# Kernel optimization log

Hardware: AMD Instinct MI355X
Metric: run time of the kernel (lower is better)

Reference implementation:

```python
import jax, jax.numpy as jnp
import numpy as np

DIM = 4096
N_HEADS = 32
N_KV_HEADS = 8
HEAD_DIM = DIM // N_HEADS  # 128
N_REP = N_HEADS // N_KV_HEADS  # 4
FFN_HIDDEN = 11008
EPS = 1e-6
B, S = 4, 2048


def rms_norm(x, gamma):
    # x: [b, s, d]
    var = jnp.mean(x * x, axis=-1, keepdims=True)
    return gamma * (x * jax.lax.rsqrt(var + EPS))


def apply_rope(x, cos, sin):
    # x: [b, s, h, d]; cos/sin: [s, d/2]. Complex rotation on (even, odd) pairs.
    x2 = x.reshape(*x.shape[:-1], HEAD_DIM // 2, 2)
    x0, x1 = x2[..., 0], x2[..., 1]
    c = cos[None, :, None, :]
    s = sin[None, :, None, :]
    r0 = x0 * c - x1 * s
    r1 = x0 * s + x1 * c
    return jnp.stack([r0, r1], axis=-1).reshape(x.shape)


def setup_inputs() -> dict:
    key = jax.random.key(0)
    ks = jax.random.split(key, 16)
    sc = 0.02
    inp = {
        "x": jax.random.normal(ks[0], (B, S, DIM), dtype=jnp.float32),
        "freqs": jax.random.uniform(ks[1], (S, HEAD_DIM // 2), dtype=jnp.float32) * (2 * np.pi),
        "start_pos": 0,
        "gamma_attn": jnp.ones((DIM,), jnp.float32),
        "gamma_ffn": jnp.ones((DIM,), jnp.float32),
        "wq_w": sc * jax.random.normal(ks[2], (N_HEADS * HEAD_DIM, DIM), jnp.float32),
        "wq_b": jnp.zeros((N_HEADS * HEAD_DIM,), jnp.float32),
        "wk_w": sc * jax.random.normal(ks[3], (N_KV_HEADS * HEAD_DIM, DIM), jnp.float32),
        "wk_b": jnp.zeros((N_KV_HEADS * HEAD_DIM,), jnp.float32),
        "wv_w": sc * jax.random.normal(ks[4], (N_KV_HEADS * HEAD_DIM, DIM), jnp.float32),
        "wv_b": jnp.zeros((N_KV_HEADS * HEAD_DIM,), jnp.float32),
        "wo_w": sc * jax.random.normal(ks[5], (DIM, N_HEADS * HEAD_DIM), jnp.float32),
        "wo_b": jnp.zeros((DIM,), jnp.float32),
        "w1_w": sc * jax.random.normal(ks[6], (FFN_HIDDEN, DIM), jnp.float32),
        "w3_w": sc * jax.random.normal(ks[7], (FFN_HIDDEN, DIM), jnp.float32),
        "w2_w": sc * jax.random.normal(ks[8], (DIM, FFN_HIDDEN), jnp.float32),
    }
    return inp


def reference(x, freqs, start_pos, gamma_attn, gamma_ffn,
              wq_w, wq_b, wk_w, wk_b, wv_w, wv_b, wo_w, wo_b,
              w1_w, w3_w, w2_w):
    cos, sin = jnp.cos(freqs), jnp.sin(freqs)

    # --- attention sublayer ---
    xn = rms_norm(x, gamma_attn)
    xq = (xn @ wq_w.T + wq_b).reshape(B, S, N_HEADS, HEAD_DIM)
    xk = (xn @ wk_w.T + wk_b).reshape(B, S, N_KV_HEADS, HEAD_DIM)
    xv = (xn @ wv_w.T + wv_b).reshape(B, S, N_KV_HEADS, HEAD_DIM)
    xq = apply_rope(xq, cos, sin)
    xk = apply_rope(xk, cos, sin)

    # KV cache: start_pos=0 prefill -> cache slice [0:start_pos+S] == current xk/xv
    keys = jnp.repeat(xk, N_REP, axis=2)   # [b, s, n_heads, d]
    values = jnp.repeat(xv, N_REP, axis=2)

    scores = jnp.einsum('bqhd,bkhd->bhqk', xq, keys) / np.sqrt(HEAD_DIM)
    probs = jax.nn.softmax(scores.astype(jnp.float32), axis=-1).astype(xq.dtype)
    attn = jnp.einsum('bhqk,bkhd->bqhd', probs, values).reshape(B, S, DIM)
    h = x + attn @ wo_w.T + wo_b

    # --- FFN sublayer (LLaMA SwiGLU) ---
    hn = rms_norm(h, gamma_ffn)
    ff = (jax.nn.silu(hn @ w1_w.T) * (hn @ w3_w.T)) @ w2_w.T
    return h + ff
```

## Files before the change

### kernel.cpp

```cpp
#include <hip/hip_runtime.h>
#include <hip/hip_bf16.h>

#define DIM   4096
#define NH    32
#define NKV   8
#define HD    128
#define FFNH  11008
#define BATCH 4
#define SEQ   2048
#define MTOT  (BATCH*SEQ)

using bf16x8_t = __attribute__((ext_vector_type(8))) short;
using f32x4_t  = __attribute__((ext_vector_type(4))) float;

typedef const __attribute__((address_space(1))) unsigned int GlbU32;
typedef __attribute__((address_space(3))) unsigned int LdsU32;

__device__ __forceinline__ unsigned short f2b(float f) {
  union { float f; unsigned int u; } v; v.f = f;
  return (unsigned short)((v.u + 0x7fffu + ((v.u >> 16) & 1u)) >> 16);
}
__device__ __forceinline__ float b2f(unsigned short b) {
  union { unsigned int u; float f; } v; v.u = ((unsigned int)b) << 16;
  return v.f;
}
__device__ __forceinline__ void gll16(const void* g, void* l) {
  __builtin_amdgcn_global_load_lds((GlbU32*)g, (LdsU32*)l, 16, 0, 0);
}

#define VM8  asm volatile("s_waitcnt vmcnt(8)" ::: "memory")
#define VM4M asm volatile("s_waitcnt vmcnt(4)" ::: "memory")
#define VM0  asm volatile("s_waitcnt vmcnt(0)" ::: "memory")

__global__ __launch_bounds__(256)
void cvt_bf16_k(const float* __restrict__ src, unsigned short* __restrict__ dst)
{
  const size_t i = ((size_t)blockIdx.x * 256 + threadIdx.x) * 8;
  const float4 a = *(const float4*)&src[i];
  const float4 b = *(const float4*)&src[i + 4];
  union { int4 v; unsigned short u[8]; } o;
  o.u[0] = f2b(a.x); o.u[1] = f2b(a.y); o.u[2] = f2b(a.z); o.u[3] = f2b(a.w);
  o.u[4] = f2b(b.x); o.u[5] = f2b(b.y); o.u[6] = f2b(b.z); o.u[7] = f2b(b.w);
  *(int4*)&dst[i] = o.v;
}

__global__ __launch_bounds__(256)
void rmsnorm_k(const float* __restrict__ X, const float* __restrict__ gamma,
               unsigned short* __restrict__ Y)
{
  const int row = blockIdx.x, t = threadIdx.x;
  const float* xr = X + (size_t)row * DIM;
  float4 v[4];
  float ss = 0.f;
#pragma unroll
  for (int p = 0; p < 4; ++p) {
    v[p] = *(const float4*)&xr[p * 1024 + t * 4];
    ss += v[p].x*v[p].x + v[p].y*v[p].y + v[p].z*v[p].z + v[p].w*v[p].w;
  }
#pragma unroll
  for (int off = 32; off >= 1; off >>= 1) ss += __shfl_xor(ss, off, 64);
  __shared__ float red[4];
  if ((t & 63) == 0) red[t >> 6] = ss;
  __syncthreads();
  const float tot = red[0] + red[1] + red[2] + red[3];
  const float rn = rsqrtf(tot * (1.f / DIM) + 1e-6f);
  unsigned short* yr = Y + (size_t)row * DIM;
#pragma unroll
  for (int p = 0; p < 4; ++p) {
    const float4 gv = *(const float4*)&gamma[p * 1024 + t * 4];
    short4 o;
    o.x = (short)f2b(v[p].x * gv.x * rn);
    o.y = (short)f2b(v[p].y * gv.y * rn);
    o.z = (short)f2b(v[p].z * gv.z * rn);
    o.w = (short)f2b(v[p].w * gv.w * rn);
    *(short4*)&yr[p * 1024 + t * 4] = o;
  }
}

template<int NHT>
__global__ __launch_bounds__(256)
void rope_k(unsigned short* __restrict__ buf, const float* __restrict__ fr)
{
  const int u = blockIdx.x * 256 + threadIdx.x;
  const int per_row = NHT * 16;
  const int row  = u / per_row;
  const int rem  = u - row * per_row;
  const int head = rem >> 4;
  const int i4   = (rem & 15) << 2;
  const int s    = row & (SEQ - 1);
  unsigned short* p = buf + (size_t)row * (NHT * HD) + head * HD + i4 * 2;
  union { int4 v; unsigned short u16[8]; } d;
  d.v = *(const int4*)p;
  const float4 f = *(const float4*)&fr[s * 64 + i4];
  const float fa[4] = {f.x, f.y, f.z, f.w};
#pragma unroll
  for (int i = 0; i < 4; ++i) {
    float sn, c;
    __sincosf(fa[i], &sn, &c);
    const float x0 = b2f(d.u16[2*i]), x1 = b2f(d.u16[2*i+1]);
    d.u16[2*i]   = f2b(x0 * c - x1 * sn);
    d.u16[2*i+1] = f2b(x0 * sn + x1 * c);
  }
  *(int4*)p = d.v;
}

template<int MODE>
__global__ __launch_bounds__(512)
void gemm256(const unsigned short* __restrict__ A,
             const unsigned short* __restrict__ W,
             const unsigned short* __restrict__ W3p,
             const float* __restrict__ bias,
             const float* res,
             float* outF,
             unsigned short* __restrict__ outH,
             const unsigned short* __restrict__ wkp,
             const unsigned short* __restrict__ wvp,
             const float* __restrict__ bkp,
             const float* __restrict__ bvp,
             unsigned short* __restrict__ okp,
             unsigned short* __restrict__ ovp,
             int K)
{
  __shared__ __align__(16) char smem[131072];
  const int t = threadIdx.x, lane = t & 63, wid = t >> 6;
  const int wr = wid >> 2, wc = wid & 3;
  const int G = gridDim.x, bid = blockIdx.x;
  const int wg = (bid & 7) * (G >> 3) + (bid >> 3);
  const int NBN = G >> 5;
  const int span = NBN << 3;
  const int tmg = wg / span, rr = wg - tmg * span;
  const int tn = rr >> 3, tm = (tmg << 3) + (rr & 7);
  const int m0 = tm << 8;
  const int NSUB = K >> 5;

  const unsigned short *P1, *P2;
  const float* bp = bias;
  unsigned short* oh = outH;
  int nloc = 0, colsN = 4096;
  if constexpr (MODE == 0) {
    const int n0 = tn << 8;
    if (n0 < 4096)      { nloc = n0;        P1 = W   + (size_t)nloc * K; bp = bias; oh = outH; colsN = 4096; }
    else if (n0 < 5120) { nloc = n0 - 4096; P1 = wkp + (size_t)nloc * K; bp = bkp;  oh = okp;  colsN = 1024; }
    else                { nloc = n0 - 5120; P1 = wvp + (size_t)nloc * K; bp = bvp;  oh = ovp;  colsN = 1024; }
    P2 = P1 + (size_t)128 * K;
  } else if constexpr (MODE == 3) {
    const int n0w = tn << 7;
    P1 = W   + (size_t)n0w * K;
    P2 = W3p + (size_t)n0w * K;
    nloc = n0w;
  } else {
    const int n0 = tn << 8;
    P1 = W + (size_t)n0 * K;
    P2 = P1 + (size_t)128 * K;
    nloc = n0;
  }

  const int r0 = t >> 2, gg = t & 3;
  const int gsw = gg ^ ((r0 >> 1) & 3);

  auto stA = [&](int sig) {
    if (sig < NSUB) {
      const int slot = sig & 3;
      gll16(A + (size_t)(m0 + r0) * K + sig * 32 + gsw * 8,
            smem + slot * 16384 + wid * 1024);
      gll16(A + (size_t)(m0 + 128 + r0) * K + sig * 32 + gsw * 8,
            smem + slot * 16384 + 8192 + wid * 1024);
    }
  };
  auto stB = [&](int sig) {
    if (sig < NSUB) {
      const int slot = sig & 3;
      gll16(P1 + (size_t)r0 * K + sig * 32 + gsw * 8,
            smem + 65536 + slot * 16384 + wid * 1024);
      gll16(P2 + (size_t)r0 * K + sig * 32 + gsw * 8,
            smem + 65536 + slot * 16384 + 8192 + wid * 1024);
    }
  };
  auto rdA = [&](int slot, int mo) -> bf16x8_t {
    const int lrow = wr * 128 + mo + (lane & 15);
    const int g = (lane >> 4) ^ ((lrow >> 1) & 3);
    return *(const bf16x8_t*)(smem + slot * 16384 + lrow * 64 + g * 16);
  };
  auto rdB = [&](int slot, int nf) -> bf16x8_t {
    const int brow = wc * 64 + nf * 16 + (lane & 15);
    const int g = (lane >> 4) ^ ((brow >> 1) & 3);
    return *(const bf16x8_t*)(smem + 65536 + slot * 16384 + brow * 64 + g * 16);
  };

  f32x4_t acc[8][4];
#pragma unroll
  for (int i = 0; i < 8; ++i)
#pragma unroll
    for (int j = 0; j < 4; ++j) acc[i][j] = (f32x4_t)0.f;

  stA(0); stB(0); stA(1); stB(1); stA(2); stB(2);
  VM8;
  __builtin_amdgcn_s_barrier();

  for (int p = 0; p < NSUB; ++p) {
    const int slot = p & 3;
    bf16x8_t bfv[4], afv[8];
#pragma unroll
    for (int n = 0; n < 4; ++n) bfv[n] = rdB(slot, n);
#pragma unroll
    for (int m = 0; m < 8; ++m) afv[m] = rdA(slot, m * 16);
    stA(p + 3); stB(p + 3);
    __builtin_amdgcn_s_setprio(1);
#pragma unroll
    for (int m = 0; m < 8; ++m)
#pragma unroll
      for (int n = 0; n < 4; ++n)
        acc[m][n] = __builtin_amdgcn_mfma_f32_16x16x32_bf16(afv[m], bfv[n], acc[m][n], 0, 0, 0);
    __builtin_amdgcn_s_setprio(0);
    if (p < NSUB - 3)      { VM8; }
    else if (p == NSUB - 3){ VM4M; }
    else                   { VM0; }
    __builtin_amdgcn_s_barrier();
  }

  if constexpr (MODE == 0) {
#pragma unroll
    for (int ni = 0; ni < 4; ++ni) {
      const int col = nloc + wc * 64 + ni * 16 + (lane & 15);
      const float bv = bp[col];
#pragma unroll
      for (int mi = 0; mi < 8; ++mi)
#pragma unroll
        for (int r = 0; r < 4; ++r) {
          const int row = m0 + wr * 128 + mi * 16 + (lane >> 4) * 4 + r;
          oh[(size_t)row * colsN + col] = f2b(acc[mi][ni][r] + bv);
        }
    }
  } else if constexpr (MODE == 1 || MODE == 2) {
#pragma unroll
    for (int ni = 0; ni < 4; ++ni) {
      const int col = nloc + wc * 64 + ni * 16 + (lane & 15);
      float bv = 0.f;
      if constexpr (MODE == 1) bv = bias[col];
#pragma unroll
      for (int mi = 0; mi < 8; ++mi)
#pragma unroll
        for (int r = 0; r < 4; ++r) {
          const int row = m0 + wr * 128 + mi * 16 + (lane >> 4) * 4 + r;
          const size_t idx = (size_t)row * 4096 + col;
          outF[idx] = acc[mi][ni][r] + bv + res[idx];
        }
    }
  } else {
    if (wc >= 2) {
      const int widx = wr * 2 + (wc - 2);
#pragma unroll
      for (int ni = 0; ni < 4; ++ni)
#pragma unroll
        for (int mi = 0; mi < 8; ++mi)
#pragma unroll
          for (int r = 0; r < 4; ++r) {
            const int lrow = mi * 16 + (lane >> 4) * 4 + r;
            const int ncol = ni * 16 + (lane & 15);
            *(unsigned short*)(smem + widx * 16384 + lrow * 128 + ncol * 2) =
                f2b(acc[mi][ni][r]);
          }
    }
    __syncthreads();
    if (wc < 2) {
      const int widx = wr * 2 + wc;
#pragma unroll
      for (int ni = 0; ni < 4; ++ni)
#pragma unroll
        for (int mi = 0; mi < 8; ++mi)
#pragma unroll
          for (int r = 0; r < 4; ++r) {
            const int lrow = mi * 16 + (lane >> 4) * 4 + r;
            const int ncol = ni * 16 + (lane & 15);
            const float s3 = b2f(*(const unsigned short*)(smem + widx * 16384 + lrow * 128 + ncol * 2));
            const float s1 = acc[mi][ni][r];
            const float sig = 1.f / (1.f + __expf(-s1));
            const int row = m0 + wr * 128 + lrow;
            outH[(size_t)row * FFNH + nloc + wc * 64 + ncol] = f2b(s1 * sig * s3);
          }
    }
  }
}

__global__ __launch_bounds__(256, 3)
void attn_k(const unsigned short* __restrict__ Q, const unsigned short* __restrict__ Kb,
            const unsigned short* __restrict__ Vb, unsigned short* __restrict__ O,
            const float* __restrict__ woS, unsigned short* __restrict__ woD,
            const float* __restrict__ w1S, unsigned short* __restrict__ w1D,
            const float* __restrict__ w3S, unsigned short* __restrict__ w3D)
{
  __shared__ unsigned short Ks[4][4096];
  __shared__ unsigned short Vt[2][4096];
  __shared__ unsigned short Ps[2560];
  const int t = threadIdx.x, lane = t & 63, wid = t >> 6;
  const int bx = blockIdx.x;
  const int qt = bx & 31, h = (bx >> 5) & 31, b = bx >> 10;
  const int kvh = h >> 2;
  const float rs = 0.08838834764831845f;
  constexpr int NPAIR = SEQ / 64;

  const int q0 = wid * 16;
  const int qc = lane & 15;

  bf16x8_t qf[4];
  {
    const unsigned short* qrow = Q + (size_t)(b * SEQ + qt * 64 + q0 + qc) * DIM
                                   + h * HD + (lane >> 4) * 8;
#pragma unroll
    for (int ks = 0; ks < 4; ++ks) qf[ks] = *(const bf16x8_t*)(qrow + ks * 32);
  }

  const unsigned short* Kbase = Kb + (size_t)(b * SEQ) * (NKV * HD) + kvh * HD;
  const unsigned short* Vbase = Vb + (size_t)(b * SEQ) * (NKV * HD) + kvh * HD;

  auto stK = [&](int kt, int slot) {
#pragma unroll
    for (int oo = 0; oo < 2; ++oo) {
      const int o = wid * 2 + oo;
      const int row = o * 4 + (lane >> 4);
      const int gl  = (lane & 15) ^ (row & 7);
      gll16(Kbase + (size_t)(kt * 32 + row) * (NKV * HD) + gl * 8, &Ks[slot][o * 512]);
    }
  };
  const int kv = t >> 3, dc = (t & 7) << 4;
  const int colv = kv ^ ((t & 3) << 3);
  auto ldV = [&](int kt, int4& lo, int4& hi) {
    const unsigned short* gp = Vbase + (size_t)(kt * 32 + kv) * (NKV * HD) + dc;
    lo = *(const int4*)gp;
    hi = *(const int4*)(gp + 8);
  };
  auto wrV = [&](int slot, int4 vlo, int4 vhi) {
    union { int4 v; unsigned short u[8]; } lo, hi;
    lo.v = vlo; hi.v = vhi;
#pragma unroll
    for (int j = 0; j < 8; ++j) Vt[slot][(dc + j) * 32 + colv] = lo.u[j];
#pragma unroll
    for (int j = 0; j < 8; ++j) Vt[slot][(dc + 8 + j) * 32 + colv] = hi.u[j];
  };

  int4 a0l, a0h, a1l, a1h, b0l, b0h, b1l, b1h;
  stK(0, 0); ldV(0, a0l, a0h); stK(1, 1); ldV(1, a1l, a1h);
  stK(2, 2); ldV(2, b0l, b0h); stK(3, 3); ldV(3, b1l, b1h);

  f32x4_t oa[8];
#pragma unroll
  for (int i = 0; i < 8; ++i) oa[i] = (f32x4_t)0.f;
  float mrun = -1e30f, lrun = 0.f;
  const int pbase = wid * 640 + qc * 40;
  const int pwr   = pbase + (lane >> 4) * 4;

  auto pack2 = [&](float x, float y) -> unsigned int {
    return (unsigned int)f2b(x) | ((unsigned int)f2b(y) << 16);
  };

  auto pairIter = [&](int p, int sb, int4& l0, int4& h0, int4& l1, int4& h1) {
    if (p == NPAIR - 1) { VM0; } else { VM8; }
    wrV(0, l0, h0);
    wrV(1, l1, h1);
    asm volatile("s_waitcnt lgkmcnt(0)" ::: "memory");
    __builtin_amdgcn_s_barrier();

    f32x4_t st[4];
    st[0] = (f32x4_t)0.f; st[1] = (f32x4_t)0.f;
    st[2] = (f32x4_t)0.f; st[3] = (f32x4_t)0.f;
    const int kr0 = qc, kr1 = 16 + qc;
    __builtin_amdgcn_s_setprio(1);
#pragma unroll
    for (int ks = 0; ks < 4; ++ks) {
      const bf16x8_t k00 = *(const bf16x8_t*)&Ks[sb][(kr0 * 128 + ks * 32 + (lane >> 4) * 8) ^ ((kr0 & 7) << 3)];
      st[0] = __builtin_amdgcn_mfma_f32_16x16x32_bf16(k00, qf[ks], st[0], 0, 0, 0);
      const bf16x8_t k01 = *(const bf16x8_t*)&Ks[sb][(kr1 * 128 + ks * 32 + (lane >> 4) * 8) ^ ((kr1 & 7) << 3)];
      st[1] = __builtin_amdgcn_mfma_f32_16x16x32_bf16(k01, qf[ks], st[1], 0, 0, 0);
      const bf16x8_t k10 = *(const bf16x8_t*)&Ks[sb + 1][(kr0 * 128 + ks * 32 + (lane >> 4) * 8) ^ ((kr0 & 7) << 3)];
      st[2] = __builtin_amdgcn_mfma_f32_16x16x32_bf16(k10, qf[ks], st[2], 0, 0, 0);
      const bf16x8_t k11 = *(const bf16x8_t*)&Ks[sb + 1][(kr1 * 128 + ks * 32 + (lane >> 4) * 8) ^ ((kr1 & 7) << 3)];
      st[3] = __builtin_amdgcn_mfma_f32_16x16x32_bf16(k11, qf[ks], st[3], 0, 0, 0);
    }
    __builtin_amdgcn_s_setprio(0);

    float mx01 = fmaxf(fmaxf(st[0][0], st[0][1]), fmaxf(st[0][2], st[0][3]));
    float mx23 = fmaxf(fmaxf(st[1][0], st[1][1]), fmaxf(st[1][2], st[1][3]));
    float mx45 = fmaxf(fmaxf(st[2][0], st[2][1]), fmaxf(st[2][2], st[2][3]));
    float mx67 = fmaxf(fmaxf(st[3][0], st[3][1]), fmaxf(st[3][2], st[3][3]));
    float pm = fmaxf(fmaxf(mx01, mx23), fmaxf(mx45, mx67)) * rs;
    pm = fmaxf(pm, __shfl_xor(pm, 16, 64));
    pm = fmaxf(pm, __shfl_xor(pm, 32, 64));

    const int grow = __any(pm > mrun);
    if (grow) {
      const float mnew = fmaxf(mrun, pm);
      const float corr = __expf(mrun - mnew);
      mrun = mnew;
      lrun *= corr;
      float c4[4];
#pragma unroll
      for (int r = 0; r < 4; ++r) c4[r] = __shfl(corr, (lane >> 4) * 4 + r, 16);
#pragma unroll
      for (int i = 0; i < 8; ++i)
#pragma unroll
        for (int r = 0; r < 4; ++r) oa[i][r] *= c4[r];
    }

    float ssum = 0.f;
#pragma unroll
    for (int tt = 0; tt < 4; ++tt)
#pragma unroll
      for (int r = 0; r < 4; ++r) {
        st[tt][r] = __expf(st[tt][r] * rs - mrun);
        ssum += st[tt][r];
      }
    ssum += __shfl_xor(ssum, 16, 64);
    ssum += __shfl_xor(ssum, 32, 64);
    lrun += ssum;

    *(unsigned int*)&Ps[pwr]      = pack2(st[0][0], st[0][1]);
    *(unsigned int*)&Ps[pwr + 2]  = pack2(st[0][2], st[0][3]);
    *(unsigned int*)&Ps[pwr + 16] = pack2(st[1][0], st[1][1]);
    *(unsigned int*)&Ps[pwr + 18] = pack2(st[1][2], st[1][3]);
    const bf16x8_t pa0 = *(const bf16x8_t*)&Ps[pbase + (lane >> 4) * 8];
    asm volatile("s_waitcnt lgkmcnt(0)" ::: "memory");
    *(unsigned int*)&Ps[pwr]      = pack2(st[2][0], st[2][1]);
    *(unsigned int*)&Ps[pwr + 2]  = pack2(st[2][2], st[2][3]);
    *(unsigned int*)&Ps[pwr + 16] = pack2(st[3][0], st[3][1]);
    *(unsigned int*)&Ps[pwr + 18] = pack2(st[3][2], st[3][3]);
    const bf16x8_t pa1 = *(const bf16x8_t*)&Ps[pbase + (lane >> 4) * 8];

    __builtin_amdgcn_s_setprio(1);
#pragma unroll
    for (int nt2 = 0; nt2 < 8; ++nt2) {
      const bf16x8_t vf0 = *(const bf16x8_t*)&Vt[0][(nt2 * 16 + (lane & 15)) * 32 + (((lane >> 4) ^ (nt2 & 3)) << 3)];
      oa[nt2] = __builtin_amdgcn_mfma_f32_16x16x32_bf16(pa0, vf0, oa[nt2], 0, 0, 0);
      const bf16x8_t vf1 = *(const bf16x8_t*)&Vt[1][(nt2 * 16 + (lane & 15)) * 32 + (((lane >> 4) ^ (nt2 & 3)) << 3)];
      oa[nt2] = __builtin_amdgcn_mfma_f32_16x16x32_bf16(pa1, vf1, oa[nt2], 0, 0, 0);
    }
    __builtin_amdgcn_s_setprio(0);
    __builtin_amdgcn_s_barrier();
    if (p + 2 < NPAIR) {
      stK(2 * p + 4, sb);     ldV(2 * p + 4, l0, h0);
      stK(2 * p + 5, sb + 1); ldV(2 * p + 5, l1, h1);
    }
  };

  for (int j = 0; j < NPAIR / 2; ++j) {
    pairIter(2 * j,     0, a0l, a0h, a1l, a1h);
    pairIter(2 * j + 1, 2, b0l, b0h, b1l, b1h);
  }

  float inv[4];
#pragma unroll
  for (int r = 0; r < 4; ++r) inv[r] = 1.f / __shfl(lrun, (lane >> 4) * 4 + r, 16);
#pragma unroll
  for (int nt2 = 0; nt2 < 8; ++nt2) {
    const int col = h * HD + nt2 * 16 + (lane & 15);
#pragma unroll
    for (int r = 0; r < 4; ++r) {
      const int row = qt * 64 + q0 + (lane >> 4) * 4 + r;
      O[(size_t)(b * SEQ + row) * DIM + col] = f2b(oa[nt2][r] * inv[r]);
    }
  }

  {
    const size_t gt = (size_t)bx * 256 + t;
    for (size_t e = gt * 8; e < 106954752ull; e += 8ull * 1048576ull) {
      const float* src; unsigned short* dst; size_t o;
      if (e < 16777216ull)      { src = woS; dst = woD; o = e; }
      else if (e < 61865984ull) { src = w1S; dst = w1D; o = e - 16777216ull; }
      else                      { src = w3S; dst = w3D; o = e - 61865984ull; }
      const float4 va = *(const float4*)&src[o];
      const float4 vb = *(const float4*)&src[o + 4];
      union { int4 v; unsigned short u[8]; } ov;
      ov.u[0] = f2b(va.x); ov.u[1] = f2b(va.y); ov.u[2] = f2b(va.z); ov.u[3] = f2b(va.w);
      ov.u[4] = f2b(vb.x); ov.u[5] = f2b(vb.y); ov.u[6] = f2b(vb.z); ov.u[7] = f2b(vb.w);
      *(int4*)&dst[o] = ov.v;
    }
  }
}

extern "C" void kernel_launch(void* const* d_in, const int* in_sizes, int n_in,
                              void* d_out, int out_size, void* d_ws, size_t ws_size,
                              hipStream_t stream)
{
  (void)in_sizes; (void)n_in; (void)out_size; (void)ws_size;
  const float* x   = (const float*)d_in[0];
  const float* fr  = (const float*)d_in[1];
  const float* ga  = (const float*)d_in[3];
  const float* gf  = (const float*)d_in[4];
  const float* wq  = (const float*)d_in[5];
  const float* wqb = (const float*)d_in[6];
  const float* wk  = (const float*)d_in[7];
  const float* wkb = (const float*)d_in[8];
  const float* wv  = (const float*)d_in[9];
  const float* wvb = (const float*)d_in[10];
  const float* wo  = (const float*)d_in[11];
  const float* wob = (const float*)d_in[12];
  const float* w1  = (const float*)d_in[13];
  const float* w3  = (const float*)d_in[14];
  const float* w2  = (const float*)d_in[15];
  float* out = (float*)d_out;

  constexpr size_t MB = 1ull << 20;
  char* ws = (char*)d_ws;
  unsigned short* xn = (unsigned short*)(ws);
  unsigned short* qb = (unsigned short*)(ws + 64*MB);
  unsigned short* kb = (unsigned short*)(ws + 128*MB);
  unsigned short* vb = (unsigned short*)(ws + 144*MB);
  unsigned short* ao = (unsigned short*)(ws + 160*MB);
  unsigned short* hn = (unsigned short*)(ws + 224*MB);
  unsigned short* g  = (unsigned short*)(ws);
  unsigned short* wscr = (unsigned short*)(ws + 288*MB);
  unsigned short* wqB = wscr;
  unsigned short* wkB = wscr + 16*MB;
  unsigned short* wvB = wscr + 20*MB;
  unsigned short* woB = (unsigned short*)(ws);
  unsigned short* w1B = wscr;
  unsigned short* w3B = wscr + 46*MB;
  unsigned short* w2B = wscr;

  rmsnorm_k<<<MTOT, 256, 0, stream>>>(x, ga, xn);
  cvt_bf16_k<<<(NH*HD*DIM)/2048,  256, 0, stream>>>(wq, wqB);
  cvt_bf16_k<<<(NKV*HD*DIM)/2048, 256, 0, stream>>>(wk, wkB);
  cvt_bf16_k<<<(NKV*HD*DIM)/2048, 256, 0, stream>>>(wv, wvB);
  gemm256<0><<<(MTOT/256)*((DIM+2*NKV*HD)/256), 512, 0, stream>>>(
      xn, wqB, nullptr, wqb, nullptr, nullptr, qb,
      wkB, wvB, wkb, wvb, kb, vb, DIM);
  rope_k<NH><<<(MTOT*NH*16)/256,  256, 0, stream>>>(qb, fr);
  rope_k<NKV><<<(MTOT*NKV*16)/256,256, 0, stream>>>(kb, fr);
  attn_k<<<BATCH*NH*(SEQ/64), 256, 0, stream>>>(qb, kb, vb, ao,
      wo, woB, w1, w1B, w3, w3B);
  gemm256<1><<<(MTOT/256)*(DIM/256), 512, 0, stream>>>(
      ao, woB, nullptr, wob, x, out, nullptr,
      nullptr, nullptr, nullptr, nullptr, nullptr, nullptr, DIM);
  rmsnorm_k<<<MTOT, 256, 0, stream>>>(out, gf, hn);
  gemm256<3><<<(MTOT/256)*(FFNH/128), 512, 0, stream>>>(
      hn, w1B, w3B, nullptr, nullptr, nullptr, g,
      nullptr, nullptr, nullptr, nullptr, nullptr, nullptr, DIM);
  cvt_bf16_k<<<(FFNH*DIM)/2048, 256, 0, stream>>>(w2, w2B);
  gemm256<2><<<(MTOT/256)*(DIM/256), 512, 0, stream>>>(
      g, w2B, nullptr, nullptr, out, out, nullptr,
      nullptr, nullptr, nullptr, nullptr, nullptr, nullptr, FFNH);
}
```

Before: 3.632 ms.

## Double attention query tile to 128 rows with 8 waves per block

The attention kernel now runs 512 threads (8 waves) per block covering 128 query rows instead of 64, halving the grid. Each K/V tile loaded into shared memory is reused by twice as many query rows, which cuts global K/V traffic and per-block load work; the K/V staging is respread across 512 threads with one 16-byte load each. The cost is a larger P scratch buffer, fewer blocks to fill the GPU, and a tighter register budget under the new launch bound of 4 blocks.

```diff
diff --git a/kernel.cpp b/kernel.cpp
--- a/kernel.cpp
+++ b/kernel.cpp
@@ -282,7 +282,7 @@
   }
 }
 
-__global__ __launch_bounds__(256, 3)
+__global__ __launch_bounds__(512, 4)
 void attn_k(const unsigned short* __restrict__ Q, const unsigned short* __restrict__ Kb,
             const unsigned short* __restrict__ Vb, unsigned short* __restrict__ O,
             const float* __restrict__ woS, unsigned short* __restrict__ woD,
@@ -291,10 +291,10 @@
 {
   __shared__ unsigned short Ks[4][4096];
   __shared__ unsigned short Vt[2][4096];
-  __shared__ unsigned short Ps[2560];
+  __shared__ unsigned short Ps[5120];
   const int t = threadIdx.x, lane = t & 63, wid = t >> 6;
   const int bx = blockIdx.x;
-  const int qt = bx & 31, h = (bx >> 5) & 31, b = bx >> 10;
+  const int qt = bx & 15, h = (bx >> 4) & 31, b = bx >> 9;
   const int kvh = h >> 2;
   const float rs = 0.08838834764831845f;
   constexpr int NPAIR = SEQ / 64;
@@ -304,7 +304,7 @@
 
   bf16x8_t qf[4];
   {
-    const unsigned short* qrow = Q + (size_t)(b * SEQ + qt * 64 + q0 + qc) * DIM
+    const unsigned short* qrow = Q + (size_t)(b * SEQ + qt * 128 + q0 + qc) * DIM
                                    + h * HD + (lane >> 4) * 8;
 #pragma unroll
     for (int ks = 0; ks < 4; ++ks) qf[ks] = *(const bf16x8_t*)(qrow + ks * 32);
@@ -314,33 +314,25 @@
   const unsigned short* Vbase = Vb + (size_t)(b * SEQ) * (NKV * HD) + kvh * HD;
 
   auto stK = [&](int kt, int slot) {
-#pragma unroll
-    for (int oo = 0; oo < 2; ++oo) {
-      const int o = wid * 2 + oo;
-      const int row = o * 4 + (lane >> 4);
-      const int gl  = (lane & 15) ^ (row & 7);
-      gll16(Kbase + (size_t)(kt * 32 + row) * (NKV * HD) + gl * 8, &Ks[slot][o * 512]);
-    }
-  };
-  const int kv = t >> 3, dc = (t & 7) << 4;
-  const int colv = kv ^ ((t & 3) << 3);
-  auto ldV = [&](int kt, int4& lo, int4& hi) {
-    const unsigned short* gp = Vbase + (size_t)(kt * 32 + kv) * (NKV * HD) + dc;
-    lo = *(const int4*)gp;
-    hi = *(const int4*)(gp + 8);
-  };
-  auto wrV = [&](int slot, int4 vlo, int4 vhi) {
-    union { int4 v; unsigned short u[8]; } lo, hi;
-    lo.v = vlo; hi.v = vhi;
-#pragma unroll
-    for (int j = 0; j < 8; ++j) Vt[slot][(dc + j) * 32 + colv] = lo.u[j];
-#pragma unroll
-    for (int j = 0; j < 8; ++j) Vt[slot][(dc + 8 + j) * 32 + colv] = hi.u[j];
-  };
-
-  int4 a0l, a0h, a1l, a1h, b0l, b0h, b1l, b1h;
-  stK(0, 0); ldV(0, a0l, a0h); stK(1, 1); ldV(1, a1l, a1h);
-  stK(2, 2); ldV(2, b0l, b0h); stK(3, 3); ldV(3, b1l, b1h);
+    const int row = t >> 4;
+    const int gl  = (t & 15) ^ (row & 7);
+    gll16(Kbase + (size_t)(kt * 32 + row) * (NKV * HD) + gl * 8, &Ks[slot][(size_t)t * 8]);
+  };
+  const int kv = t >> 4;
+  const int d0 = (t & 15) * 8;
+  const int colv = kv ^ (((d0 >> 4) & 3) << 3);
+  auto ldV = [&](int kt, int4& w) {
+    w = *(const int4*)(Vbase + (size_t)(kt * 32 + kv) * (NKV * HD) + d0);
+  };
+  auto wrV = [&](int slot, int4 w) {
+    union { int4 v; unsigned short u[8]; } u; u.v = w;
+#pragma unroll
+    for (int j = 0; j < 8; ++j) Vt[slot][(d0 + j) * 32 + colv] = u.u[j];
+  };
+
+  int4 a0, a1, b0, b1;
+  stK(0, 0); stK(1, 1); ldV(0, a0); ldV(1, a1);
+  stK(2, 2); stK(3, 3); ldV(2, b0); ldV(3, b1);
 
   f32x4_t oa[8];
 #pragma unroll
@@ -353,10 +345,10 @@
     return (unsigned int)f2b(x) | ((unsigned int)f2b(y) << 16);
   };
 
-  auto pairIter = [&](int p, int sb, int4& l0, int4& h0, int4& l1, int4& h1) {
-    if (p == NPAIR - 1) { VM0; } else { VM8; }
-    wrV(0, l0, h0);
-    wrV(1, l1, h1);
+  auto pairIter = [&](int p, int sb, int4& l0, int4& l1) {
+    if (p == NPAIR - 1) { VM0; } else { VM4M; }
+    wrV(0, l0);
+    wrV(1, l1);
     asm volatile("s_waitcnt lgkmcnt(0)" ::: "memory");
     __builtin_amdgcn_s_barrier();
 
@@ -436,14 +428,14 @@
     __builtin_amdgcn_s_setprio(0);
     __builtin_amdgcn_s_barrier();
     if (p + 2 < NPAIR) {
-      stK(2 * p + 4, sb);     ldV(2 * p + 4, l0, h0);
-      stK(2 * p + 5, sb + 1); ldV(2 * p + 5, l1, h1);
+      stK(2 * p + 4, sb);     stK(2 * p + 5, sb + 1);
+      ldV(2 * p + 4, l0);     ldV(2 * p + 5, l1);
     }
   };
 
   for (int j = 0; j < NPAIR / 2; ++j) {
-    pairIter(2 * j,     0, a0l, a0h, a1l, a1h);
-    pairIter(2 * j + 1, 2, b0l, b0h, b1l, b1h);
+    pairIter(2 * j,     0, a0, a1);
+    pairIter(2 * j + 1, 2, b0, b1);
   }
 
   float inv[4];
@@ -454,13 +446,13 @@
     const int col = h * HD + nt2 * 16 + (lane & 15);
 #pragma unroll
     for (int r = 0; r < 4; ++r) {
-      const int row = qt * 64 + q0 + (lane >> 4) * 4 + r;
+      const int row = qt * 128 + q0 + (lane >> 4) * 4 + r;
       O[(size_t)(b * SEQ + row) * DIM + col] = f2b(oa[nt2][r] * inv[r]);
     }
   }
 
   {
-    const size_t gt = (size_t)bx * 256 + t;
+    const size_t gt = (size_t)bx * 512 + t;
     for (size_t e = gt * 8; e < 106954752ull; e += 8ull * 1048576ull) {
       const float* src; unsigned short* dst; size_t o;
       if (e < 16777216ull)      { src = woS; dst = woD; o = e; }
@@ -525,7 +517,7 @@
       wkB, wvB, wkb, wvb, kb, vb, DIM);
   rope_k<NH><<<(MTOT*NH*16)/256,  256, 0, stream>>>(qb, fr);
   rope_k<NKV><<<(MTOT*NKV*16)/256,256, 0, stream>>>(kb, fr);
-  attn_k<<<BATCH*NH*(SEQ/64), 256, 0, stream>>>(qb, kb, vb, ao,
+  attn_k<<<BATCH*NH*(SEQ/128), 512, 0, stream>>>(qb, kb, vb, ao,
       wo, woB, w1, w1B, w3, w3B);
   gemm256<1><<<(MTOT/256)*(DIM/256), 512, 0, stream>>>(
       ao, woB, nullptr, wob, x, out, nullptr,
```

Result: faster. 3.466 ms (-4.6%).
